# Kernel tuning notes

Measured on AMD Instinct MI355X. Metric: run time of the kernel, lower is better.

Reference implementation:

```python
import jax, jax.numpy as jnp
import numpy as np

LMAX = 2
C1 = 64; C2 = 64; COUT = 64
B = 4096
SUM_RDIM = sum(3**L for L in range(LMAX + 1))   # 13
FEAT1 = C1 * SUM_RDIM                            # 832
FEAT2 = C2 * SUM_RDIM


def _enumerate_paths(Lmax):
    paths = []
    for L1 in range(Lmax + 1):
        for L2 in range(Lmax + 1):
            for k in range(min(L1, L2) + 1):
                Lout = L1 + L2 - 2 * k
                if 0 <= Lout <= Lmax:
                    paths.append((L1, L2, Lout, k, False))
            if L1 >= 1 and L2 >= 1:
                for k in range(min(L1 - 1, L2 - 1) + 1):
                    Lout = L1 + L2 - 2 * k - 1
                    if 0 <= Lout <= Lmax:
                        paths.append((L1, L2, Lout, k, True))
    return paths

PATHS = _enumerate_paths(LMAX)   # 15 paths for Lmax=2


def _path_eq(L1, L2, k, use_eps):
    # Fused equation: W[c,a,b] contracted together with the delta/eps path einsum.
    letters = list('defghijklmnopqrstuvwxyz')  # a,b,c reserved for channels
    i_idx = letters[:L1]
    j_idx = letters[L1:L1 + L2]
    for r in range(k):  # delta: contract last k indices of A with last k of B
        j_idx[L2 - k + r] = i_idx[L1 - k + r]
    i_free = i_idx[:L1 - k]
    j_free = j_idx[:L2 - k]
    eps_sub = None
    if use_eps:  # consume last free index of each side via eps_{p i j}
        p = letters[L1 + L2]
        eps_sub = p + i_free[-1] + j_free[-1]
        i_free, j_free = i_free[:-1], j_free[:-1]
        out = i_free + j_free + [p]
    else:
        out = i_free + j_free
    terms = ['cab', '...a' + ''.join(i_idx), '...b' + ''.join(j_idx)]
    if eps_sub is not None:
        terms.append(eps_sub)
    return ','.join(terms) + '->...c' + ''.join(out)


def _epsilon():
    e = np.zeros((3, 3, 3), dtype=np.float32)
    e[0, 1, 2] = e[1, 2, 0] = e[2, 0, 1] = 1.0
    e[2, 1, 0] = e[1, 0, 2] = e[0, 2, 1] = -1.0
    return jnp.asarray(e)


def _split_by_rank(x, C, Lmax):
    batch = x.shape[:-1]
    out, idx = {}, 0
    for L in range(Lmax + 1):
        d = C * 3**L
        blk = x[..., idx:idx + d]
        idx += d
        out[L] = blk.reshape(*batch, C) if L == 0 else blk.reshape(*batch, C, *((3,) * L))
    return out


def setup_inputs() -> dict:
    key = jax.random.key(0)
    k1, k2, k3 = jax.random.split(key, 3)
    x1 = jax.random.normal(k1, (B, FEAT1), dtype=jnp.float32)
    x2 = jax.random.normal(k2, (B, FEAT2), dtype=jnp.float32)
    weight = jax.random.normal(k3, (len(PATHS) * COUT * C1 * C2,), dtype=jnp.float32) * 0.02
    return {"x1": x1, "x2": x2, "weight": weight}


def reference(x1, x2, weight):
    A = _split_by_rank(x1, C1, LMAX)
    Bt = _split_by_rank(x2, C2, LMAX)
    eps = _epsilon().astype(x1.dtype)
    batch = x1.shape[:-1]
    blocks = {L: jnp.zeros((*batch, COUT) + (3,) * L, dtype=x1.dtype) for L in range(LMAX + 1)}
    wsz = COUT * C1 * C2
    for n, (L1, L2, Lout, k, use_eps) in enumerate(PATHS):
        Wp = weight[n * wsz:(n + 1) * wsz].reshape(COUT, C1, C2)
        eq = _path_eq(L1, L2, k, use_eps)
        ops = (Wp, A[L1], Bt[L2]) + ((eps,) if use_eps else ())
        blocks[Lout] = blocks[Lout] + jnp.einsum(eq, *ops, optimize='optimal')
    parts = [blocks[L].reshape(*batch, COUT * 3**L) for L in range(LMAX + 1)]
    return jnp.concatenate(parts, axis=-1)
```

## Files before the change

### kernel.cpp

```cpp
#include <hip/hip_runtime.h>
#include <cstdint>
#include <cstddef>


#define FEAT 832

typedef _Float16 half8 __attribute__((ext_vector_type(8)));
typedef float floatx16 __attribute__((ext_vector_type(16)));

struct Chunk {
  int wbase;
  int s1[3];
  int s2[3];
  unsigned short sgm[3];
  int nt;
};

__global__ void swz_w_kernel(const float* __restrict__ w, _Float16* __restrict__ o) {
  const int i = blockIdx.x * 256 + threadIdx.x;
  const int lane = i & 63;
  const int pkc  = i >> 6;
  const int cgrp = pkc & 1;
  const int ksg  = (pkc >> 1) & 255;
  const int p    = pkc >> 9;
  const int c  = cgrp * 32 + (lane & 31);
  const int k0 = ksg * 16 + (lane >> 5) * 8;
  const float* src = w + (size_t)p * 262144 + (size_t)c * 4096 + k0;
  const float4 v0 = *(const float4*)(src);
  const float4 v1 = *(const float4*)(src + 4);
  half8 h = { (_Float16)v0.x, (_Float16)v0.y, (_Float16)v0.z, (_Float16)v0.w,
              (_Float16)v1.x, (_Float16)v1.y, (_Float16)v1.z, (_Float16)v1.w };
  *(half8*)(o + (size_t)i * 8) = h;
}

__global__ __launch_bounds__(256) void xpose_kernel(
    const float* __restrict__ x1, const float* __restrict__ x2,
    _Float16* __restrict__ X1T, _Float16* __restrict__ X2T)
{
  __shared__ _Float16 T[64][66];
  const int s = blockIdx.y;
  const int which = blockIdx.z;
  const int zbase = blockIdx.x * 64;
  int offs, d, j;
  if (s == 0)      { offs = 0;   d = 1; j = 0; }
  else if (s < 4)  { offs = 64;  d = 3; j = s - 1; }
  else             { offs = 256; d = 9; j = s - 4; }
  const float* __restrict__ src = which ? x2 : x1;
  const int tid = threadIdx.x;
  const int kk = tid & 63;
  const int z4 = tid >> 6;
  #pragma unroll
  for (int i = 0; i < 16; ++i) {
    const int zz = z4 + i * 4;
    T[kk][zz] = (_Float16)src[(size_t)(zbase + zz) * FEAT + offs + kk * d + j];
  }
  __syncthreads();
  const int c = tid & 63;
  const int r4 = tid >> 6;
  if (which == 0) {
    #pragma unroll
    for (int i = 0; i < 16; ++i) {
      const int a = r4 + i * 4;
      X1T[(size_t)(s * 64 + a) * 4096 + zbase + c] = T[a][c];
    }
  } else {
    #pragma unroll
    for (int i = 0; i < 16; ++i) {
      const int zz = r4 + i * 4;
      X2T[((size_t)s * 4096 + zbase + zz) * 64 + c] = T[c][zz];
    }
  }
}

__device__ __forceinline__ half8 splat8(_Float16 h) {
  return half8{h, h, h, h, h, h, h, h};
}

template<int NT>
__device__ __forceinline__ void run_chunk(
    const Chunk C, const int zbase, const int zl, const int hf,
    const int lane, const int a0,
    const _Float16* __restrict__ Wh, const unsigned short* __restrict__ X1u,
    const _Float16* __restrict__ X2L,
    floatx16& acc0, floatx16& acc1)
{
  half8 x2r[NT][4];
  #pragma unroll
  for (int t = 0; t < NT; ++t) {
    const _Float16* row = X2L + (C.s2[t] * 64 + zl) * 72 + hf * 8;
    #pragma unroll
    for (int ks = 0; ks < 4; ++ks)
      x2r[t][ks] = *(const half8*)(row + ks * 16);
  }

  const unsigned short* xp[NT];
  #pragma unroll
  for (int t = 0; t < NT; ++t)
    xp[t] = X1u + (size_t)(C.s1[t] * 64) * 4096 + zbase + zl;

  const _Float16* __restrict__ Wq = Wh + C.wbase + lane * 8;

  half8 af[2][4];
  {
    const _Float16* w0 = Wq + (size_t)a0 * 4096;
    #pragma unroll
    for (int ks = 0; ks < 4; ++ks) {
      af[0][ks] = *(const half8*)(w0 + ks * 1024);
      af[1][ks] = *(const half8*)(w0 + ks * 1024 + 512);
    }
  }
  unsigned short sc[NT], scn[NT];
  #pragma unroll
  for (int t = 0; t < NT; ++t) {
    sc[t]  = xp[t][(size_t)a0 * 4096];
    scn[t] = xp[t][(size_t)(a0 + 1) * 4096];
  }

  const int aend = a0 + 32;
  #pragma unroll 1
  for (int a = a0; a < aend; ++a) {
    half8 sv[NT];
    #pragma unroll
    for (int t = 0; t < NT; ++t) {
      unsigned short u = (unsigned short)(sc[t] ^ C.sgm[t]);
      _Float16 h;
      __builtin_memcpy(&h, &u, 2);
      sv[t] = splat8(h);
    }
    #pragma unroll
    for (int t = 0; t < NT; ++t) sc[t] = scn[t];
    if (a + 2 < aend) {
      #pragma unroll
      for (int t = 0; t < NT; ++t) scn[t] = xp[t][(size_t)(a + 2) * 4096];
    }
    __builtin_amdgcn_s_setprio(1);
    #pragma unroll
    for (int ks = 0; ks < 4; ++ks) {
      half8 tb = sv[0] * x2r[0][ks];
      if (NT > 1) tb += sv[1] * x2r[1][ks];
      if (NT > 2) tb += sv[2] * x2r[2][ks];
      acc0 = __builtin_amdgcn_mfma_f32_32x32x16_f16(af[0][ks], tb, acc0, 0, 0, 0);
      acc1 = __builtin_amdgcn_mfma_f32_32x32x16_f16(af[1][ks], tb, acc1, 0, 0, 0);
    }
    __builtin_amdgcn_s_setprio(0);
    if (a + 1 < aend) {
      const _Float16* wn = Wq + (size_t)(a + 1) * 4096;
      #pragma unroll
      for (int ks = 0; ks < 4; ++ks) {
        af[0][ks] = *(const half8*)(wn + ks * 1024);
        af[1][ks] = *(const half8*)(wn + ks * 1024 + 512);
      }
    }
  }
}

__global__ __launch_bounds__(768) void tp_kernel(
    const _Float16* __restrict__ Wh, const unsigned short* __restrict__ X1u,
    const _Float16* __restrict__ X2Tg, float* __restrict__ out)
{
  __shared__ __align__(16) _Float16 X2L[13 * 64 * 72];
  __shared__ Chunk chs[3][7];
  __shared__ int nch_s;

  const int tid = threadIdx.x;
  const int bid = blockIdx.x;
  int g, zt;
  if (bid < 256) { const int u = (bid & 7) * 32 + (bid >> 3); g = 1 + (u >> 6); zt = u & 63; }
  else           { g = 0; zt = bid - 256; }
  const int zbase = zt * 64;
  const int wid  = tid >> 6;
  const int zg   = wid & 1;
  const int aq   = (wid >> 1) & 1;
  const int mm   = wid >> 2;
  const int a0   = aq * 32;
  const int lane = tid & 63;
  const int ln31 = lane & 31;
  const int hf   = lane >> 5;
  const int zl   = zg * 32 + ln31;

  if (tid == 0) {
    auto plane = [](int L, int j) { return L == 0 ? 0 : (L == 1 ? 1 + j : 4 + j); };
    for (int m = 0; m < 3; ++m) {
      int n = 0;
      auto add = [&](int p, int L1, int L2, int i0,int i1,int i2,
                     int j0,int j1,int j2, float s0,float s1,float s2, int nt) {
        Chunk c;
        c.wbase = p * 262144;
        const int is[3] = {i0,i1,i2}, js[3] = {j0,j1,j2};
        const float ss[3] = {s0,s1,s2};
        for (int t = 0; t < 3; ++t) {
          c.s1[t] = plane(L1, is[t]);
          c.s2[t] = plane(L2, js[t]);
          c.sgm[t] = ss[t] < 0.f ? (unsigned short)0x8000 : (unsigned short)0;
        }
        c.nt = nt;
        chs[m][n++] = c;
      };
      if (g == 0) {
        if (m == 0) {
          add(0, 0,0, 0,0,0, 0,0,0, 1,0,0, 1);
          add(5, 1,1, 0,1,2, 0,1,2, 1,1,1, 3);
          add(13,2,2, 0,1,2, 0,1,2, 1,1,1, 3);
          add(13,2,2, 3,4,5, 3,4,5, 1,1,1, 3);
          add(13,2,2, 6,7,8, 6,7,8, 1,1,1, 3);
          nch_s = n;
        }
      } else {
        const int slot = 3 * g - 2 + m;
        if (slot < 4) {
          const int mi = slot - 1, p1 = (mi+1)%3, p2 = (mi+2)%3;
          add(1, 0,1, 0,0,0, mi,0,0, 1,0,0, 1);
          add(3, 1,0, mi,0,0, 0,0,0, 1,0,0, 1);
          add(6, 1,1, p1,p2,0, p2,p1,0, 1,-1,0, 2);
          add(7, 1,2, 0,1,2, 3*mi,3*mi+1,3*mi+2, 1,1,1, 3);
          add(10,2,1, 3*mi,3*mi+1,3*mi+2, 0,1,2, 1,1,1, 3);
          add(14,2,2, 3*p1,3*p1+1,3*p1+2, 3*p2,3*p2+1,3*p2+2, 1,1,1, 3);
          add(14,2,2, 3*p2,3*p2+1,3*p2+2, 3*p1,3*p1+1,3*p1+2, -1,-1,-1, 3);
        } else {
          const int mi = slot - 4, uu = mi/3, v = mi%3, q1 = (v+1)%3, q2 = (v+2)%3;
          add(2, 0,2, 0,0,0, mi,0,0, 1,0,0, 1);
          add(4, 1,1, uu,0,0, v,0,0, 1,0,0, 1);
          add(8, 1,2, q1,q2,0, 3*uu+q2,3*uu+q1,0, 1,-1,0, 2);
          add(9, 2,0, mi,0,0, 0,0,0, 1,0,0, 1);
          add(11,2,1, 3*uu+q1,3*uu+q2,0, q2,q1,0, 1,-1,0, 2);
          add(12,2,2, 3*uu,3*uu+1,3*uu+2, 3*v,3*v+1,3*v+2, 1,1,1, 3);
        }
        nch_s = n;
      }
    }
  }

  for (int idx = tid; idx < 13 * 64 * 8; idx += 768) {
    const int s  = idx >> 9;
    const int rem = idx & 511;
    const int zz = rem >> 3;
    const int o8 = rem & 7;
    *(half8*)(X2L + (s * 64 + zz) * 72 + o8 * 8) =
        *(const half8*)(X2Tg + ((size_t)s * 4096 + zbase + zz) * 64 + o8 * 8);
  }
  __syncthreads();
  const int nch = nch_s;

  floatx16 acc0, acc1;
  #pragma unroll
  for (int r = 0; r < 16; ++r) { acc0[r] = 0.0f; acc1[r] = 0.0f; }

  if (g == 0) {
    for (int ci = mm; ci < nch; ci += 3) {
      const Chunk C = chs[0][ci];
      if (C.nt == 1)      run_chunk<1>(C, zbase, zl, hf, lane, a0, Wh, X1u, X2L, acc0, acc1);
      else if (C.nt == 2) run_chunk<2>(C, zbase, zl, hf, lane, a0, Wh, X1u, X2L, acc0, acc1);
      else                run_chunk<3>(C, zbase, zl, hf, lane, a0, Wh, X1u, X2L, acc0, acc1);
    }
  } else {
    for (int ci = 0; ci < nch; ++ci) {
      const Chunk C = chs[mm][ci];
      if (C.nt == 1)      run_chunk<1>(C, zbase, zl, hf, lane, a0, Wh, X1u, X2L, acc0, acc1);
      else if (C.nt == 2) run_chunk<2>(C, zbase, zl, hf, lane, a0, Wh, X1u, X2L, acc0, acc1);
      else                run_chunk<3>(C, zbase, zl, hf, lane, a0, Wh, X1u, X2L, acc0, acc1);
    }
  }

  __syncthreads();
  float* __restrict__ Dv = (float*)X2L;
  const bool writer = (aq == 0) && (g > 0 || mm == 0);
  if (!writer) {
    const int b = ((mm * 2 + aq) * 2 + zg) * 2048;
    #pragma unroll
    for (int r = 0; r < 16; ++r) {
      Dv[b + r * 64 + lane]        = acc0[r];
      Dv[b + 1024 + r * 64 + lane] = acc1[r];
    }
  }
  __syncthreads();
  if (writer) {
    if (g > 0) {
      const int b = ((mm * 2 + 1) * 2 + zg) * 2048;
      #pragma unroll
      for (int r = 0; r < 16; ++r) {
        acc0[r] += Dv[b + r * 64 + lane];
        acc1[r] += Dv[b + 1024 + r * 64 + lane];
      }
    } else {
      #pragma unroll
      for (int m2 = 0; m2 < 3; ++m2) {
        #pragma unroll
        for (int q2 = 0; q2 < 2; ++q2) {
          if (m2 == 0 && q2 == 0) continue;
          const int b = ((m2 * 2 + q2) * 2 + zg) * 2048;
          #pragma unroll
          for (int r = 0; r < 16; ++r) {
            acc0[r] += Dv[b + r * 64 + lane];
            acc1[r] += Dv[b + 1024 + r * 64 + lane];
          }
        }
      }
    }
    const int slot = (g == 0) ? 0 : 3 * g - 2 + mm;
    int offO, dO, mO;
    if (slot == 0)      { offO = 0;   dO = 1; mO = 0; }
    else if (slot < 4)  { offO = 64;  dO = 3; mO = slot - 1; }
    else                { offO = 256; dO = 9; mO = slot - 4; }
    float* __restrict__ op = out + (size_t)(zbase + zl) * FEAT + offO + mO;
    #pragma unroll
    for (int r = 0; r < 16; ++r) {
      const int cr = (r & 3) + 8 * (r >> 2) + 4 * hf;
      op[(size_t)cr * dO]        = acc0[r];
      op[(size_t)(cr + 32) * dO] = acc1[r];
    }
  }
}

extern "C" void kernel_launch(void* const* d_in, const int* in_sizes, int n_in,
                              void* d_out, int out_size, void* d_ws, size_t ws_size,
                              hipStream_t stream) {
  const float* x1 = (const float*)d_in[0];
  const float* x2 = (const float*)d_in[1];
  const float* w  = (const float*)d_in[2];
  float* out = (float*)d_out;
  _Float16* Wh  = (_Float16*)d_ws;
  _Float16* X1T = (_Float16*)((char*)d_ws + 7864320);
  _Float16* X2T = (_Float16*)((char*)d_ws + 7864320 + 6815744);

  const int nchunks = 15 * 64 * 4096 / 8;
  hipLaunchKernelGGL(swz_w_kernel, dim3(nchunks / 256), dim3(256), 0, stream, w, Wh);
  hipLaunchKernelGGL(xpose_kernel, dim3(64, 13, 2), dim3(256), 0, stream,
                     x1, x2, X1T, X2T);
  hipLaunchKernelGGL(tp_kernel, dim3(320), dim3(768), 0, stream,
                     Wh, (const unsigned short*)X1T, X2T, out);
}
```

Measured before the change: 464.1 us.

## Split waves by output-channel half instead of reduction half to drop LDS reduction

```diff
diff --git a/kernel.cpp b/kernel.cpp
--- a/kernel.cpp
+++ b/kernel.cpp
@@ -79,10 +79,10 @@
 template<int NT>
 __device__ __forceinline__ void run_chunk(
     const Chunk C, const int zbase, const int zl, const int hf,
-    const int lane, const int a0,
+    const int lane, const int cg,
     const _Float16* __restrict__ Wh, const unsigned short* __restrict__ X1u,
     const _Float16* __restrict__ X2L,
-    floatx16& acc0, floatx16& acc1)
+    floatx16& acc)
 {
   half8 x2r[NT][4];
   #pragma unroll
@@ -98,63 +98,83 @@
   for (int t = 0; t < NT; ++t)
     xp[t] = X1u + (size_t)(C.s1[t] * 64) * 4096 + zbase + zl;
 
-  const _Float16* __restrict__ Wq = Wh + C.wbase + lane * 8;
-
-  half8 af[2][4];
-  {
-    const _Float16* w0 = Wq + (size_t)a0 * 4096;
-    #pragma unroll
-    for (int ks = 0; ks < 4; ++ks) {
-      af[0][ks] = *(const half8*)(w0 + ks * 1024);
-      af[1][ks] = *(const half8*)(w0 + ks * 1024 + 512);
-    }
+  const _Float16* __restrict__ Wq = Wh + C.wbase + cg * 512 + lane * 8;
+
+  half8 afE[4], afO[4];
+  #pragma unroll
+  for (int ks = 0; ks < 4; ++ks) {
+    afE[ks] = *(const half8*)(Wq + ks * 1024);
+    afO[ks] = *(const half8*)(Wq + 4096 + ks * 1024);
   }
   unsigned short sc[NT], scn[NT];
   #pragma unroll
   for (int t = 0; t < NT; ++t) {
-    sc[t]  = xp[t][(size_t)a0 * 4096];
-    scn[t] = xp[t][(size_t)(a0 + 1) * 4096];
-  }
-
-  const int aend = a0 + 32;
+    sc[t]  = xp[t][0];
+    scn[t] = xp[t][4096];
+  }
+
   #pragma unroll 1
-  for (int a = a0; a < aend; ++a) {
-    half8 sv[NT];
-    #pragma unroll
-    for (int t = 0; t < NT; ++t) {
-      unsigned short u = (unsigned short)(sc[t] ^ C.sgm[t]);
-      _Float16 h;
-      __builtin_memcpy(&h, &u, 2);
-      sv[t] = splat8(h);
-    }
-    #pragma unroll
-    for (int t = 0; t < NT; ++t) sc[t] = scn[t];
-    if (a + 2 < aend) {
-      #pragma unroll
-      for (int t = 0; t < NT; ++t) scn[t] = xp[t][(size_t)(a + 2) * 4096];
-    }
-    __builtin_amdgcn_s_setprio(1);
-    #pragma unroll
-    for (int ks = 0; ks < 4; ++ks) {
-      half8 tb = sv[0] * x2r[0][ks];
-      if (NT > 1) tb += sv[1] * x2r[1][ks];
-      if (NT > 2) tb += sv[2] * x2r[2][ks];
-      acc0 = __builtin_amdgcn_mfma_f32_32x32x16_f16(af[0][ks], tb, acc0, 0, 0, 0);
-      acc1 = __builtin_amdgcn_mfma_f32_32x32x16_f16(af[1][ks], tb, acc1, 0, 0, 0);
-    }
-    __builtin_amdgcn_s_setprio(0);
-    if (a + 1 < aend) {
-      const _Float16* wn = Wq + (size_t)(a + 1) * 4096;
+  for (int a = 0; a < 64; a += 2) {
+    {
+      half8 sv[NT];
+      #pragma unroll
+      for (int t = 0; t < NT; ++t) {
+        unsigned short u = (unsigned short)(sc[t] ^ C.sgm[t]);
+        _Float16 h; __builtin_memcpy(&h, &u, 2);
+        sv[t] = splat8(h);
+      }
+      if (a + 2 < 64) {
+        #pragma unroll
+        for (int t = 0; t < NT; ++t) sc[t] = xp[t][(size_t)(a + 2) * 4096];
+      }
+      __builtin_amdgcn_s_setprio(1);
       #pragma unroll
       for (int ks = 0; ks < 4; ++ks) {
-        af[0][ks] = *(const half8*)(wn + ks * 1024);
-        af[1][ks] = *(const half8*)(wn + ks * 1024 + 512);
-      }
-    }
-  }
-}
-
-__global__ __launch_bounds__(768) void tp_kernel(
+        half8 tb = sv[0] * x2r[0][ks];
+        if (NT > 1) tb += sv[1] * x2r[1][ks];
+        if (NT > 2) tb += sv[2] * x2r[2][ks];
+        acc = __builtin_amdgcn_mfma_f32_32x32x16_f16(afE[ks], tb, acc, 0, 0, 0);
+      }
+      __builtin_amdgcn_s_setprio(0);
+      if (a + 2 < 64) {
+        const _Float16* wn = Wq + (size_t)(a + 2) * 4096;
+        #pragma unroll
+        for (int ks = 0; ks < 4; ++ks)
+          afE[ks] = *(const half8*)(wn + ks * 1024);
+      }
+    }
+    {
+      half8 sv[NT];
+      #pragma unroll
+      for (int t = 0; t < NT; ++t) {
+        unsigned short u = (unsigned short)(scn[t] ^ C.sgm[t]);
+        _Float16 h; __builtin_memcpy(&h, &u, 2);
+        sv[t] = splat8(h);
+      }
+      if (a + 3 < 64) {
+        #pragma unroll
+        for (int t = 0; t < NT; ++t) scn[t] = xp[t][(size_t)(a + 3) * 4096];
+      }
+      __builtin_amdgcn_s_setprio(1);
+      #pragma unroll
+      for (int ks = 0; ks < 4; ++ks) {
+        half8 tb = sv[0] * x2r[0][ks];
+        if (NT > 1) tb += sv[1] * x2r[1][ks];
+        if (NT > 2) tb += sv[2] * x2r[2][ks];
+        acc = __builtin_amdgcn_mfma_f32_32x32x16_f16(afO[ks], tb, acc, 0, 0, 0);
+      }
+      __builtin_amdgcn_s_setprio(0);
+      if (a + 3 < 64) {
+        const _Float16* wn = Wq + (size_t)(a + 3) * 4096;
+        #pragma unroll
+        for (int ks = 0; ks < 4; ++ks)
+          afO[ks] = *(const half8*)(wn + ks * 1024);
+      }
+    }
+  }
+}
+
+__global__ __launch_bounds__(768, 3) void tp_kernel(
     const _Float16* __restrict__ Wh, const unsigned short* __restrict__ X1u,
     const _Float16* __restrict__ X2Tg, float* __restrict__ out)
 {
@@ -170,9 +190,8 @@
   const int zbase = zt * 64;
   const int wid  = tid >> 6;
   const int zg   = wid & 1;
-  const int aq   = (wid >> 1) & 1;
+  const int cg   = (wid >> 1) & 1;
   const int mm   = wid >> 2;
-  const int a0   = aq * 32;
   const int lane = tid & 63;
   const int ln31 = lane & 31;
   const int hf   = lane >> 5;
@@ -241,72 +260,61 @@
   __syncthreads();
   const int nch = nch_s;
 
-  floatx16 acc0, acc1;
-  #pragma unroll
-  for (int r = 0; r < 16; ++r) { acc0[r] = 0.0f; acc1[r] = 0.0f; }
+  floatx16 acc;
+  #pragma unroll
+  for (int r = 0; r < 16; ++r) acc[r] = 0.0f;
 
   if (g == 0) {
     for (int ci = mm; ci < nch; ci += 3) {
       const Chunk C = chs[0][ci];
-      if (C.nt == 1)      run_chunk<1>(C, zbase, zl, hf, lane, a0, Wh, X1u, X2L, acc0, acc1);
-      else if (C.nt == 2) run_chunk<2>(C, zbase, zl, hf, lane, a0, Wh, X1u, X2L, acc0, acc1);
-      else                run_chunk<3>(C, zbase, zl, hf, lane, a0, Wh, X1u, X2L, acc0, acc1);
+      if (C.nt == 1)      run_chunk<1>(C, zbase, zl, hf, lane, cg, Wh, X1u, X2L, acc);
+      else if (C.nt == 2) run_chunk<2>(C, zbase, zl, hf, lane, cg, Wh, X1u, X2L, acc);
+      else                run_chunk<3>(C, zbase, zl, hf, lane, cg, Wh, X1u, X2L, acc);
     }
   } else {
     for (int ci = 0; ci < nch; ++ci) {
       const Chunk C = chs[mm][ci];
-      if (C.nt == 1)      run_chunk<1>(C, zbase, zl, hf, lane, a0, Wh, X1u, X2L, acc0, acc1);
-      else if (C.nt == 2) run_chunk<2>(C, zbase, zl, hf, lane, a0, Wh, X1u, X2L, acc0, acc1);
-      else                run_chunk<3>(C, zbase, zl, hf, lane, a0, Wh, X1u, X2L, acc0, acc1);
-    }
-  }
-
-  __syncthreads();
-  float* __restrict__ Dv = (float*)X2L;
-  const bool writer = (aq == 0) && (g > 0 || mm == 0);
-  if (!writer) {
-    const int b = ((mm * 2 + aq) * 2 + zg) * 2048;
-    #pragma unroll
-    for (int r = 0; r < 16; ++r) {
-      Dv[b + r * 64 + lane]        = acc0[r];
-      Dv[b + 1024 + r * 64 + lane] = acc1[r];
-    }
-  }
-  __syncthreads();
-  if (writer) {
-    if (g > 0) {
-      const int b = ((mm * 2 + 1) * 2 + zg) * 2048;
-      #pragma unroll
-      for (int r = 0; r < 16; ++r) {
-        acc0[r] += Dv[b + r * 64 + lane];
-        acc1[r] += Dv[b + 1024 + r * 64 + lane];
-      }
-    } else {
-      #pragma unroll
-      for (int m2 = 0; m2 < 3; ++m2) {
-        #pragma unroll
-        for (int q2 = 0; q2 < 2; ++q2) {
-          if (m2 == 0 && q2 == 0) continue;
-          const int b = ((m2 * 2 + q2) * 2 + zg) * 2048;
-          #pragma unroll
-          for (int r = 0; r < 16; ++r) {
-            acc0[r] += Dv[b + r * 64 + lane];
-            acc1[r] += Dv[b + 1024 + r * 64 + lane];
-          }
-        }
-      }
-    }
-    const int slot = (g == 0) ? 0 : 3 * g - 2 + mm;
+      if (C.nt == 1)      run_chunk<1>(C, zbase, zl, hf, lane, cg, Wh, X1u, X2L, acc);
+      else if (C.nt == 2) run_chunk<2>(C, zbase, zl, hf, lane, cg, Wh, X1u, X2L, acc);
+      else                run_chunk<3>(C, zbase, zl, hf, lane, cg, Wh, X1u, X2L, acc);
+    }
+  }
+
+  if (g > 0) {
+    const int slot = 3 * g - 2 + mm;
     int offO, dO, mO;
-    if (slot == 0)      { offO = 0;   dO = 1; mO = 0; }
-    else if (slot < 4)  { offO = 64;  dO = 3; mO = slot - 1; }
-    else                { offO = 256; dO = 9; mO = slot - 4; }
+    if (slot < 4) { offO = 64;  dO = 3; mO = slot - 1; }
+    else          { offO = 256; dO = 9; mO = slot - 4; }
     float* __restrict__ op = out + (size_t)(zbase + zl) * FEAT + offO + mO;
     #pragma unroll
     for (int r = 0; r < 16; ++r) {
-      const int cr = (r & 3) + 8 * (r >> 2) + 4 * hf;
-      op[(size_t)cr * dO]        = acc0[r];
-      op[(size_t)(cr + 32) * dO] = acc1[r];
+      const int cr = cg * 32 + (r & 3) + 8 * (r >> 2) + 4 * hf;
+      op[(size_t)cr * dO] = acc[r];
+    }
+  } else {
+    __syncthreads();
+    float* __restrict__ Dv = (float*)X2L;
+    if (mm > 0) {
+      const int b = (((mm - 1) * 2 + cg) * 2 + zg) * 1024;
+      #pragma unroll
+      for (int r = 0; r < 16; ++r)
+        Dv[b + r * 64 + lane] = acc[r];
+    }
+    __syncthreads();
+    if (mm == 0) {
+      #pragma unroll
+      for (int m2 = 1; m2 < 3; ++m2) {
+        const int b = (((m2 - 1) * 2 + cg) * 2 + zg) * 1024;
+        #pragma unroll
+        for (int r = 0; r < 16; ++r)
+          acc[r] += Dv[b + r * 64 + lane];
+      }
+      float* __restrict__ op = out + (size_t)(zbase + zl) * FEAT;
+      #pragma unroll
+      for (int r = 0; r < 16; ++r) {
+        const int cr = cg * 32 + (r & 3) + 8 * (r >> 2) + 4 * hf;
+        op[cr] = acc[r];
+      }
     }
   }
 }
```

New measurement: 450.4 us. 3.0% less time.
